# Kernel optimization log

Measured on AMD Instinct MI355X. Metric: run time of the kernel, lower is better.

The kernel has to match this reference:

```python
import jax, jax.numpy as jnp
import numpy as np

NF, NC, LENGTH, BATCH = 64, 16, 2048, 256
WEIGHT_BI, WEIGHT_L2 = 0.01, 0.01
BETA = 2.5     # temporal soft-min/max sharpness (TemporalOperator beta=2.5)
KAPPA = 10.0   # logical soft-min/max sharpness (avm approximation)
EPSN = 1e-12


def setup_inputs() -> dict:
    key = jax.random.key(0)
    ks = jax.random.split(key, 11)
    x = jax.random.normal(ks[0], (BATCH, LENGTH, 2), dtype=jnp.float32)
    t1 = jax.random.uniform(ks[1], (NF,), minval=0.0, maxval=float(LENGTH // 2), dtype=jnp.float32)
    t2 = jax.random.uniform(ks[2], (NF,), minval=float(LENGTH // 2), maxval=float(LENGTH), dtype=jnp.float32)
    a = jax.random.uniform(ks[3], (NF,), dtype=jnp.float32)
    b = jax.random.uniform(ks[4], (NF,), dtype=jnp.float32)
    p1 = jax.random.uniform(ks[5], (NC, NF), dtype=jnp.float32)
    p2 = jax.random.uniform(ks[6], (1, NC), dtype=jnp.float32)
    tvar_temporal = jax.random.uniform(ks[7], (NF,), dtype=jnp.float32)
    tvar_logical1 = jax.random.uniform(ks[8], (NC,), dtype=jnp.float32)
    tvar_logical2 = jax.random.uniform(ks[9], (1,), dtype=jnp.float32)
    eps = jnp.full((1,), 0.1, dtype=jnp.float32)
    return dict(x=x, t1=t1, t2=t2, a=a, b=b, p1=p1, p2=p2,
                tvar_temporal=tvar_temporal, tvar_logical1=tvar_logical1,
                tvar_logical2=tvar_logical2, eps=eps)


def _ste(v, v_new):
    # torch clamps parameter .data under no_grad -> value changes, grad is identity
    return v + jax.lax.stop_gradient(v_new - v)


def _wsel(r, logw, sharp):
    # weighted soft-max (sharp>0) / soft-min (sharp<0) along last axis
    s = jax.nn.softmax(sharp * r + logw, axis=-1)
    return jnp.sum(s * r, axis=-1)


def reference(x, t1, t2, a, b, p1, p2, tvar_temporal, tvar_logical1, tvar_logical2, eps):
    # --- in-place parameter maintenance (clamp under no_grad in torch) ---
    p1 = _ste(p1, jnp.clip(p1, 0.0, 1.0))
    p2 = _ste(p2, jnp.clip(p2, 0.0, 1.0))
    tvt = _ste(tvar_temporal, jnp.clip(tvar_temporal, 0.0, 1.0))
    tvl1 = _ste(tvar_logical1, jnp.clip(tvar_logical1, 0.0, 1.0))
    tvl2 = _ste(tvar_logical2, jnp.clip(tvar_logical2, 0.0, 1.0))
    t1c = jnp.clip(t1, 0.0, LENGTH - 1.0)
    t2c = jnp.clip(t2, 0.0, LENGTH - 1.0)
    t1c = jnp.where(t1c >= t2c - 1.0, t2c - 1.0, t1c)
    t1u = _ste(t1, t1c)
    t2u = _ste(t2, t2c)

    # --- predicates (vectorized over all nf features; dim = i % 2) ---
    dims = jnp.arange(NF) % 2
    rp = a[None, None, :] * x[:, :, dims] - b[None, None, :]     # [B, T, NF]
    rp = jnp.transpose(rp, (0, 2, 1))                             # [B, NF, T]

    # --- temporal operators: smooth window [t1, t2] + soft min/max over time ---
    tg = jnp.arange(LENGTH, dtype=x.dtype)
    w = jax.nn.sigmoid(BETA * (tg[None, :] - t1u[:, None])) * \
        jax.nn.sigmoid(BETA * (t2u[:, None] - tg[None, :]))       # [NF, T]
    logw = jnp.log(w + EPSN)[None]                                # [1, NF, T]
    rmax = _wsel(rp, logw, BETA)                                  # eventually  [B, NF]
    rmin = _wsel(rp, logw, -BETA)                                 # always      [B, NF]
    r1 = tvt[None, :] * rmax + (1.0 - tvt[None, :]) * rmin        # [B, NF]

    # --- logical layer 1: weighted soft OR/AND over features, per clause ---
    logp1 = jnp.log(p1 + EPSN)[None]                              # [1, NC, NF]
    r1e = r1[:, None, :]                                          # [B, NC, NF]
    r_or = _wsel(r1e, logp1, KAPPA)
    r_and = _wsel(r1e, logp1, -KAPPA)
    r2 = tvl1[None, :] * r_or + (1.0 - tvl1[None, :]) * r_and     # [B, NC]

    # --- logical layer 2: combine clauses ---
    logp2 = jnp.log(p2[0] + EPSN)[None]                           # [1, NC]
    r_or2 = _wsel(r2, logp2, KAPPA)
    r_and2 = _wsel(r2, logp2, -KAPPA)
    r = tvl2[0] * r_or2 + (1.0 - tvl2[0]) * r_and2                # [B]

    # --- regularizers ---
    bi = WEIGHT_BI * (jnp.sum(tvt * (1.0 - tvt)) + jnp.sum(tvl1 * (1.0 - tvl1)) +
                      jnp.sum(tvl2 * (1.0 - tvl2)) + jnp.sum(p1 * (1.0 - p1)) +
                      jnp.sum(p2 * (1.0 - p2)))
    l2 = WEIGHT_L2 * (jnp.sum(p1 * p1) + jnp.sum(p2 * p2))
    reg = bi + l2
    return r, reg
```

## Files before the change

### kernel.cpp

```cpp
#include <hip/hip_runtime.h>
#include <math.h>

#define NF 64
#define NC 16
#define LEN 2048
#define BATCH 256
#define BETA 2.5f
#define KAPPA 10.0f
#define EPSN 1e-12f
#define LOG2E 1.4426950408889634f

#define TPB 256
#define NQ (TPB / NF)
#define SPLIT 8
#define HALF (LEN / SPLIT)
#define CHUNK (HALF / NQ)
#define NS (SPLIT * NQ)

#define MTPB 1024
#define MNQ (MTPB / NF)
#define CHUNK_MONO (LEN / MNQ)

__device__ __forceinline__ float clip01(float v) { return fminf(fmaxf(v, 0.0f), 1.0f); }

__device__ __forceinline__ float fexp2(float x) {
#if __has_builtin(__builtin_amdgcn_exp2f)
    return __builtin_amdgcn_exp2f(x);
#else
    return exp2f(x);
#endif
}

#define LW_BLOCKS ((NF * LEN / 4) / 256)

__global__ __launch_bounds__(256) void lw_reg_kernel(
    const float* __restrict__ t1, const float* __restrict__ t2,
    const float* __restrict__ p1, const float* __restrict__ p2,
    const float* __restrict__ tvt, const float* __restrict__ tvl1,
    const float* __restrict__ tvl2, float4* __restrict__ lwT4,
    float* __restrict__ out) {
    const int bid = blockIdx.x;
    const int tid = threadIdx.x;

    if (bid == LW_BLOCKS) {
        __shared__ float red[256];
        float acc = 0.0f;
        for (int i = tid; i < NC * NF; i += 256) {
            float p = clip01(p1[i]);
            acc += 0.01f * (p * (1.0f - p)) + 0.01f * (p * p);
        }
        if (tid < NC) {
            float p = clip01(p2[tid]);
            acc += 0.01f * (p * (1.0f - p)) + 0.01f * (p * p);
        }
        if (tid < NF) {
            float c = clip01(tvt[tid]);
            acc += 0.01f * (c * (1.0f - c));
        }
        if (tid < NC) {
            float c = clip01(tvl1[tid]);
            acc += 0.01f * (c * (1.0f - c));
        }
        if (tid == 0) {
            float c = clip01(tvl2[0]);
            acc += 0.01f * (c * (1.0f - c));
        }
        red[tid] = acc;
        __syncthreads();
        for (int s = 128; s > 0; s >>= 1) {
            if (tid < s) red[tid] += red[tid + s];
            __syncthreads();
        }
        if (tid == 0) out[BATCH] = red[0];
        return;
    }

    int idx = bid * 256 + tid;
    int f = idx & (NF - 1);
    int g = idx >> 6;
    float t1c = fminf(fmaxf(t1[f], 0.0f), (float)(LEN - 1));
    float t2c = fminf(fmaxf(t2[f], 0.0f), (float)(LEN - 1));
    t1c = fminf(t1c, t2c - 1.0f);
    float4 r;
#pragma unroll
    for (int j = 0; j < 4; ++j) {
        float t = (float)(4 * g + j);
        float su = 1.0f / (1.0f + __expf(-BETA * (t - t1c)));
        float sv = 1.0f / (1.0f + __expf(-BETA * (t2c - t)));
        ((float*)&r)[j] = __log2f(su * sv + EPSN);
    }
    lwT4[idx] = r;
}

__global__ __launch_bounds__(TPB) void main_split(
    const float* __restrict__ x, const float* __restrict__ av,
    const float4* __restrict__ lwT4, float4* __restrict__ part) {
    const int b = blockIdx.x >> 3;
    const int h = blockIdx.x & 7;
    const int tid = threadIdx.x;
    const int f = tid & (NF - 1);
    const int q = tid >> 6;
    const int ch = f & 1;

    const float A2 = (BETA * LOG2E) * av[f];

    const int t0 = h * HALF + q * CHUNK;
    const float* xp = x + (size_t)b * (LEN * 2) + 2 * t0 + ch;
    const float4* lw4 = lwT4 + (t0 >> 2) * NF + f;

    float Sp0 = 0.f, Xp0 = 0.f, Sm0 = 0.f, Xm0 = 0.f;
    float Sp1 = 0.f, Xp1 = 0.f, Sm1 = 0.f, Xm1 = 0.f;
#pragma unroll 4
    for (int g = 0; g < CHUNK / 4; ++g) {
        float4 lw = lw4[g * NF];
        float x0 = xp[8 * g + 0];
        float x1 = xp[8 * g + 2];
        float x2 = xp[8 * g + 4];
        float x3 = xp[8 * g + 6];
        float e;
        e = fexp2(fmaf(A2, x0, lw.x));  Sp0 += e; Xp0 = fmaf(e, x0, Xp0);
        e = fexp2(fmaf(-A2, x0, lw.x)); Sm0 += e; Xm0 = fmaf(e, x0, Xm0);
        e = fexp2(fmaf(A2, x1, lw.y));  Sp1 += e; Xp1 = fmaf(e, x1, Xp1);
        e = fexp2(fmaf(-A2, x1, lw.y)); Sm1 += e; Xm1 = fmaf(e, x1, Xm1);
        e = fexp2(fmaf(A2, x2, lw.z));  Sp0 += e; Xp0 = fmaf(e, x2, Xp0);
        e = fexp2(fmaf(-A2, x2, lw.z)); Sm0 += e; Xm0 = fmaf(e, x2, Xm0);
        e = fexp2(fmaf(A2, x3, lw.w));  Sp1 += e; Xp1 = fmaf(e, x3, Xp1);
        e = fexp2(fmaf(-A2, x3, lw.w)); Sm1 += e; Xm1 = fmaf(e, x3, Xm1);
    }

    part[((size_t)b * NS + (h * NQ + q)) * NF + f] =
        make_float4(Sp0 + Sp1, Xp0 + Xp1, Sm0 + Sm1, Xm0 + Xm1);
}

__global__ __launch_bounds__(64) void finish_kernel(
    const float4* __restrict__ part, const float* __restrict__ av,
    const float* __restrict__ bv, const float* __restrict__ p1,
    const float* __restrict__ p2, const float* __restrict__ tvt_,
    const float* __restrict__ tvl1_, const float* __restrict__ tvl2_,
    float* __restrict__ out) {
    __shared__ float r1s[NF];
    __shared__ float r2s[NC];

    const int b = blockIdx.x;
    const int l = threadIdx.x;
    const float KL = KAPPA * LOG2E;

    float ax = 0.f, ay = 0.f, az = 0.f, aw = 0.f;
    const float4* pb = part + (size_t)b * NS * NF;
#pragma unroll
    for (int s = 0; s < NS; ++s) {
        float4 v = pb[s * NF + l];
        ax += v.x; ay += v.y; az += v.z; aw += v.w;
    }
    {
        float af = av[l], bf = bv[l];
        float tvt = clip01(tvt_[l]);
        float rmax = af * (ay / ax);
        float rmin = af * (aw / az);
        r1s[l] = tvt * rmax + (1.0f - tvt) * rmin - bf;
    }

    {
        const int c = l & 15;
        const int j = l >> 4;
        float so = 0.f, wo = 0.f, sa = 0.f, wa = 0.f;
#pragma unroll
        for (int i = 0; i < 16; ++i) {
            int ff = j * 16 + i;
            float r1v = r1s[ff];
            float lg = __log2f(clip01(p1[c * NF + ff]) + EPSN);
            float z = KL * r1v;
            float eo = fexp2(z + lg);
            float ea = fexp2(lg - z);
            so += eo; wo = fmaf(eo, r1v, wo);
            sa += ea; wa = fmaf(ea, r1v, wa);
        }
#pragma unroll
        for (int d = 16; d < 64; d <<= 1) {
            so += __shfl_xor(so, d);
            wo += __shfl_xor(wo, d);
            sa += __shfl_xor(sa, d);
            wa += __shfl_xor(wa, d);
        }
        if (l < NC) {
            float tvl1 = clip01(tvl1_[l]);
            r2s[l] = tvl1 * (wo / so) + (1.0f - tvl1) * (wa / sa);
        }
    }

    if (l == 0) {
        float so = 0.f, wo = 0.f, sa = 0.f, wa = 0.f;
#pragma unroll
        for (int c = 0; c < NC; ++c) {
            float lg = __log2f(clip01(p2[c]) + EPSN);
            float r2v = r2s[c];
            float z = KL * r2v;
            float eo = fexp2(z + lg);
            float ea = fexp2(lg - z);
            so += eo; wo = fmaf(eo, r2v, wo);
            sa += ea; wa = fmaf(ea, r2v, wa);
        }
        float tvl2 = clip01(tvl2_[0]);
        out[b] = tvl2 * (wo / so) + (1.0f - tvl2) * (wa / sa);
    }
}

__global__ __launch_bounds__(MTPB) void main_mono(
    const float* __restrict__ x, const float* __restrict__ av,
    const float* __restrict__ bv,
    const float* __restrict__ t1g, const float* __restrict__ t2g,
    const float* __restrict__ p1, const float* __restrict__ p2,
    const float* __restrict__ tvt_, const float* __restrict__ tvl1_,
    const float* __restrict__ tvl2_, float* __restrict__ out) {
    __shared__ float4 redQ[MNQ][NF];
    __shared__ float lp[NC][NF];
    __shared__ float r1s[NF];
    __shared__ float r2s[NC];

    const int b = blockIdx.x;
    const int tid = threadIdx.x;
    const int f = tid & (NF - 1);
    const int q = tid >> 6;
    const float B2 = BETA * LOG2E;
    const float KL = KAPPA * LOG2E;

    const float a = av[f];
    const float bb = bv[f];
    const int ch = f & 1;

    float t1c = fminf(fmaxf(t1g[f], 0.0f), (float)(LEN - 1));
    float t2c = fminf(fmaxf(t2g[f], 0.0f), (float)(LEN - 1));
    t1c = fminf(t1c, t2c - 1.0f);

    const int t0 = q * CHUNK_MONO;
    const float* xp = x + (size_t)b * (LEN * 2) + 2 * t0 + ch;
    float sp = 0.f, wp = 0.f, sm = 0.f, wm = 0.f;
#pragma unroll 8
    for (int k = 0; k < CHUNK_MONO; ++k) {
        int t = t0 + k;
        float su = 1.0f / (1.0f + __expf(-BETA * ((float)t - t1c)));
        float sv = 1.0f / (1.0f + __expf(-BETA * (t2c - (float)t)));
        float lw2 = __log2f(su * sv + EPSN);
        float xv = xp[2 * k];
        float rp = fmaf(a, xv, -bb);
        float ep = fexp2(fmaf(B2, rp, lw2));
        float em = fexp2(fmaf(-B2, rp, lw2));
        sp += ep; wp = fmaf(ep, rp, wp);
        sm += em; wm = fmaf(em, rp, wm);
    }
    redQ[q][f] = make_float4(sp, wp, sm, wm);
    {
        float pv = clip01(p1[tid]);
        ((float*)lp)[tid] = __log2f(pv + EPSN);
    }
    __syncthreads();

    if (q == 0) {
        float Sp = 0.f, Wp = 0.f, Sm = 0.f, Wm = 0.f;
#pragma unroll
        for (int j = 0; j < MNQ; ++j) {
            float4 v = redQ[j][f];
            Sp += v.x; Wp += v.y; Sm += v.z; Wm += v.w;
        }
        float tvt = clip01(tvt_[f]);
        r1s[f] = tvt * (Wp / Sp) + (1.0f - tvt) * (Wm / Sm);
    }
    __syncthreads();

    if (tid < NC) {
        const int c = tid;
        float so = 0.f, wo = 0.f, sa = 0.f, wa = 0.f;
#pragma unroll
        for (int ff = 0; ff < NF; ++ff) {
            float r1v = r1s[ff];
            float z = KL * r1v;
            float lg = lp[c][ff];
            float eo = fexp2(z + lg);
            float ea = fexp2(lg - z);
            so += eo; wo = fmaf(eo, r1v, wo);
            sa += ea; wa = fmaf(ea, r1v, wa);
        }
        float tvl1 = clip01(tvl1_[c]);
        r2s[c] = tvl1 * (wo / so) + (1.0f - tvl1) * (wa / sa);
    }
    __syncthreads();

    if (tid == 0) {
        float so = 0.f, wo = 0.f, sa = 0.f, wa = 0.f;
#pragma unroll
        for (int c = 0; c < NC; ++c) {
            float lg = __log2f(clip01(p2[c]) + EPSN);
            float r2v = r2s[c];
            float z = KL * r2v;
            float eo = fexp2(z + lg);
            float ea = fexp2(lg - z);
            so += eo; wo = fmaf(eo, r2v, wo);
            sa += ea; wa = fmaf(ea, r2v, wa);
        }
        float tvl2 = clip01(tvl2_[0]);
        out[b] = tvl2 * (wo / so) + (1.0f - tvl2) * (wa / sa);
    }
}

__global__ void reg_kernel(const float* __restrict__ p1, const float* __restrict__ p2,
                           const float* __restrict__ tvt, const float* __restrict__ tvl1,
                           const float* __restrict__ tvl2, float* __restrict__ out) {
    __shared__ float red[256];
    int tid = threadIdx.x;
    float acc = 0.0f;
    for (int i = tid; i < NC * NF; i += 256) {
        float p = clip01(p1[i]);
        acc += 0.01f * (p * (1.0f - p)) + 0.01f * (p * p);
    }
    if (tid < NC) {
        float p = clip01(p2[tid]);
        acc += 0.01f * (p * (1.0f - p)) + 0.01f * (p * p);
    }
    if (tid < NF) {
        float c = clip01(tvt[tid]);
        acc += 0.01f * (c * (1.0f - c));
    }
    if (tid < NC) {
        float c = clip01(tvl1[tid]);
        acc += 0.01f * (c * (1.0f - c));
    }
    if (tid == 0) {
        float c = clip01(tvl2[0]);
        acc += 0.01f * (c * (1.0f - c));
    }
    red[tid] = acc;
    __syncthreads();
    for (int s = 128; s > 0; s >>= 1) {
        if (tid < s) red[tid] += red[tid + s];
        __syncthreads();
    }
    if (tid == 0) out[BATCH] = red[0];
}

extern "C" void kernel_launch(void* const* d_in, const int* in_sizes, int n_in,
                              void* d_out, int out_size, void* d_ws, size_t ws_size,
                              hipStream_t stream) {
    const float* x    = (const float*)d_in[0];
    const float* t1   = (const float*)d_in[1];
    const float* t2   = (const float*)d_in[2];
    const float* a    = (const float*)d_in[3];
    const float* bv   = (const float*)d_in[4];
    const float* p1   = (const float*)d_in[5];
    const float* p2   = (const float*)d_in[6];
    const float* tvt  = (const float*)d_in[7];
    const float* tvl1 = (const float*)d_in[8];
    const float* tvl2 = (const float*)d_in[9];
    float* out = (float*)d_out;

    const size_t lw_bytes = (size_t)(NF * LEN) * sizeof(float);
    const size_t part_bytes = (size_t)BATCH * NS * NF * sizeof(float4);

    if (d_ws && ws_size >= lw_bytes + part_bytes) {
        float4* lwT4 = (float4*)d_ws;
        float4* part = (float4*)((char*)d_ws + lw_bytes);
        lw_reg_kernel<<<LW_BLOCKS + 1, 256, 0, stream>>>(t1, t2, p1, p2, tvt, tvl1,
                                                         tvl2, lwT4, out);
        main_split<<<BATCH * SPLIT, TPB, 0, stream>>>(x, a, lwT4, part);
        finish_kernel<<<BATCH, 64, 0, stream>>>(part, a, bv, p1, p2, tvt, tvl1,
                                                tvl2, out);
    } else {
        main_mono<<<BATCH, MTPB, 0, stream>>>(x, a, bv, t1, t2, p1, p2,
                                              tvt, tvl1, tvl2, out);
        reg_kernel<<<1, 256, 0, stream>>>(p1, p2, tvt, tvl1, tvl2, out);
    }
}
```

Baseline: 27.44 us.

## Fuse weight precompute, split reduction and finish into one per-batch kernel

Replaces the three-kernel pipeline (precomputed log-window table, split partial sums in a global workspace, separate finish pass) with a single kernel of 1024 threads per batch row. The time-window weight is computed inline as the reciprocal of a product of two sigmoid denominators. The plus and minus exponentials are factored into exp2(A*x) and its reciprocal, which cuts the transcendentals per element. Partial sums are reduced in shared memory, and the regularizer is folded into block 0. This removes two launches and the workspace traffic. In exchange it drops EPSN inside the log, launches only 256 blocks, and risks overflow or precision loss from the factored exponent.

New measurement: 26.90 us. 2.0% less time.

```diff
diff --git a/kernel.cpp b/kernel.cpp
--- a/kernel.cpp
+++ b/kernel.cpp
@@ -10,16 +10,9 @@
 #define EPSN 1e-12f
 #define LOG2E 1.4426950408889634f
 
-#define TPB 256
+#define TPB 1024
 #define NQ (TPB / NF)
-#define SPLIT 8
-#define HALF (LEN / SPLIT)
-#define CHUNK (HALF / NQ)
-#define NS (SPLIT * NQ)
-
-#define MTPB 1024
-#define MNQ (MTPB / NF)
-#define CHUNK_MONO (LEN / MNQ)
+#define CHUNK (LEN / NQ)
 
 __device__ __forceinline__ float clip01(float v) { return fminf(fmaxf(v, 0.0f), 1.0f); }
 
@@ -31,125 +24,117 @@
 #endif
 }
 
-#define LW_BLOCKS ((NF * LEN / 4) / 256)
-
-__global__ __launch_bounds__(256) void lw_reg_kernel(
-    const float* __restrict__ t1, const float* __restrict__ t2,
-    const float* __restrict__ p1, const float* __restrict__ p2,
-    const float* __restrict__ tvt, const float* __restrict__ tvl1,
-    const float* __restrict__ tvl2, float4* __restrict__ lwT4,
+__device__ __forceinline__ float frcp(float x) {
+#if __has_builtin(__builtin_amdgcn_rcpf)
+    return __builtin_amdgcn_rcpf(x);
+#else
+    return 1.0f / x;
+#endif
+}
+
+__global__ __launch_bounds__(TPB) void fused_kernel(
+    const float* __restrict__ x, const float* __restrict__ t1g,
+    const float* __restrict__ t2g, const float* __restrict__ av,
+    const float* __restrict__ bv, const float* __restrict__ p1,
+    const float* __restrict__ p2, const float* __restrict__ tvt_,
+    const float* __restrict__ tvl1_, const float* __restrict__ tvl2_,
     float* __restrict__ out) {
-    const int bid = blockIdx.x;
-    const int tid = threadIdx.x;
-
-    if (bid == LW_BLOCKS) {
-        __shared__ float red[256];
-        float acc = 0.0f;
-        for (int i = tid; i < NC * NF; i += 256) {
-            float p = clip01(p1[i]);
-            acc += 0.01f * (p * (1.0f - p)) + 0.01f * (p * p);
-        }
-        if (tid < NC) {
-            float p = clip01(p2[tid]);
-            acc += 0.01f * (p * (1.0f - p)) + 0.01f * (p * p);
-        }
-        if (tid < NF) {
-            float c = clip01(tvt[tid]);
-            acc += 0.01f * (c * (1.0f - c));
-        }
-        if (tid < NC) {
-            float c = clip01(tvl1[tid]);
-            acc += 0.01f * (c * (1.0f - c));
-        }
-        if (tid == 0) {
-            float c = clip01(tvl2[0]);
-            acc += 0.01f * (c * (1.0f - c));
-        }
-        red[tid] = acc;
-        __syncthreads();
-        for (int s = 128; s > 0; s >>= 1) {
-            if (tid < s) red[tid] += red[tid + s];
-            __syncthreads();
-        }
-        if (tid == 0) out[BATCH] = red[0];
-        return;
-    }
-
-    int idx = bid * 256 + tid;
-    int f = idx & (NF - 1);
-    int g = idx >> 6;
-    float t1c = fminf(fmaxf(t1[f], 0.0f), (float)(LEN - 1));
-    float t2c = fminf(fmaxf(t2[f], 0.0f), (float)(LEN - 1));
-    t1c = fminf(t1c, t2c - 1.0f);
-    float4 r;
-#pragma unroll
-    for (int j = 0; j < 4; ++j) {
-        float t = (float)(4 * g + j);
-        float su = 1.0f / (1.0f + __expf(-BETA * (t - t1c)));
-        float sv = 1.0f / (1.0f + __expf(-BETA * (t2c - t)));
-        ((float*)&r)[j] = __log2f(su * sv + EPSN);
-    }
-    lwT4[idx] = r;
-}
-
-__global__ __launch_bounds__(TPB) void main_split(
-    const float* __restrict__ x, const float* __restrict__ av,
-    const float4* __restrict__ lwT4, float4* __restrict__ part) {
-    const int b = blockIdx.x >> 3;
-    const int h = blockIdx.x & 7;
+    __shared__ float4 redQ[NQ][NF];
+    __shared__ float r1s[NF];
+    __shared__ float r2s[NC];
+
+    const int b = blockIdx.x;
     const int tid = threadIdx.x;
     const int f = tid & (NF - 1);
     const int q = tid >> 6;
     const int ch = f & 1;
 
-    const float A2 = (BETA * LOG2E) * av[f];
-
-    const int t0 = h * HALF + q * CHUNK;
-    const float* xp = x + (size_t)b * (LEN * 2) + 2 * t0 + ch;
-    const float4* lw4 = lwT4 + (t0 >> 2) * NF + f;
+    const float B2 = BETA * LOG2E;
+    const float KL = KAPPA * LOG2E;
+
+    const float a = av[f];
+    const float A2 = B2 * a;
+
+    float t1c = fminf(fmaxf(t1g[f], 0.0f), (float)(LEN - 1));
+    float t2c = fminf(fmaxf(t2g[f], 0.0f), (float)(LEN - 1));
+    t1c = fminf(t1c, t2c - 1.0f);
+    const float c1 = B2 * t1c;
+    const float c2 = -B2 * t2c;
+
+    const int t0 = q * CHUNK;
+    const float4* xp4 = (const float4*)(x + (size_t)b * (LEN * 2) + 2 * t0);
 
     float Sp0 = 0.f, Xp0 = 0.f, Sm0 = 0.f, Xm0 = 0.f;
     float Sp1 = 0.f, Xp1 = 0.f, Sm1 = 0.f, Xm1 = 0.f;
 #pragma unroll 4
-    for (int g = 0; g < CHUNK / 4; ++g) {
-        float4 lw = lw4[g * NF];
-        float x0 = xp[8 * g + 0];
-        float x1 = xp[8 * g + 2];
-        float x2 = xp[8 * g + 4];
-        float x3 = xp[8 * g + 6];
-        float e;
-        e = fexp2(fmaf(A2, x0, lw.x));  Sp0 += e; Xp0 = fmaf(e, x0, Xp0);
-        e = fexp2(fmaf(-A2, x0, lw.x)); Sm0 += e; Xm0 = fmaf(e, x0, Xm0);
-        e = fexp2(fmaf(A2, x1, lw.y));  Sp1 += e; Xp1 = fmaf(e, x1, Xp1);
-        e = fexp2(fmaf(-A2, x1, lw.y)); Sm1 += e; Xm1 = fmaf(e, x1, Xm1);
-        e = fexp2(fmaf(A2, x2, lw.z));  Sp0 += e; Xp0 = fmaf(e, x2, Xp0);
-        e = fexp2(fmaf(-A2, x2, lw.z)); Sm0 += e; Xm0 = fmaf(e, x2, Xm0);
-        e = fexp2(fmaf(A2, x3, lw.w));  Sp1 += e; Xp1 = fmaf(e, x3, Xp1);
-        e = fexp2(fmaf(-A2, x3, lw.w)); Sm1 += e; Xm1 = fmaf(e, x3, Xm1);
-    }
-
-    part[((size_t)b * NS + (h * NQ + q)) * NF + f] =
-        make_float4(Sp0 + Sp1, Xp0 + Xp1, Sm0 + Sm1, Xm0 + Xm1);
-}
-
-__global__ __launch_bounds__(64) void finish_kernel(
-    const float4* __restrict__ part, const float* __restrict__ av,
-    const float* __restrict__ bv, const float* __restrict__ p1,
-    const float* __restrict__ p2, const float* __restrict__ tvt_,
-    const float* __restrict__ tvl1_, const float* __restrict__ tvl2_,
-    float* __restrict__ out) {
-    __shared__ float r1s[NF];
-    __shared__ float r2s[NC];
-
-    const int b = blockIdx.x;
-    const int l = threadIdx.x;
-    const float KL = KAPPA * LOG2E;
-
+    for (int k2 = 0; k2 < CHUNK / 2; ++k2) {
+        float4 v = xp4[k2];
+        float xa = ch ? v.y : v.x;
+        float xb = ch ? v.w : v.z;
+        float tfa = (float)(t0 + 2 * k2);
+        float tfb = tfa + 1.0f;
+
+        {
+            float g1 = fmaf(-B2, tfa, c1);
+            float g2 = fmaf(B2, tfa, c2);
+            float den = (1.0f + fexp2(g1)) * (1.0f + fexp2(g2));
+            float w = frcp(den);
+            float P = fexp2(A2 * xa);
+            float Pm = frcp(P);
+            float tp = P * w, tm = Pm * w;
+            Sp0 += tp; Xp0 = fmaf(tp, xa, Xp0);
+            Sm0 += tm; Xm0 = fmaf(tm, xa, Xm0);
+        }
+        {
+            float g1 = fmaf(-B2, tfb, c1);
+            float g2 = fmaf(B2, tfb, c2);
+            float den = (1.0f + fexp2(g1)) * (1.0f + fexp2(g2));
+            float w = frcp(den);
+            float P = fexp2(A2 * xb);
+            float Pm = frcp(P);
+            float tp = P * w, tm = Pm * w;
+            Sp1 += tp; Xp1 = fmaf(tp, xb, Xp1);
+            Sm1 += tm; Xm1 = fmaf(tm, xb, Xm1);
+        }
+    }
+
+    redQ[q][f] = make_float4(Sp0 + Sp1, Xp0 + Xp1, Sm0 + Sm1, Xm0 + Xm1);
+
+    if (b == 0 && q == NQ - 1) {
+        const int l = f;
+        float acc = 0.0f;
+#pragma unroll
+        for (int i = 0; i < 16; ++i) {
+            float p = clip01(p1[i * NF + l]);
+            acc += 0.01f * (p * (1.0f - p)) + 0.01f * (p * p);
+        }
+        {
+            float c = clip01(tvt_[l]);
+            acc += 0.01f * (c * (1.0f - c));
+        }
+        if (l < NC) {
+            float p = clip01(p2[l]);
+            acc += 0.01f * (p * (1.0f - p)) + 0.01f * (p * p);
+            float c = clip01(tvl1_[l]);
+            acc += 0.01f * (c * (1.0f - c));
+        }
+        if (l == 0) {
+            float c = clip01(tvl2_[0]);
+            acc += 0.01f * (c * (1.0f - c));
+        }
+#pragma unroll
+        for (int d = 1; d < 64; d <<= 1) acc += __shfl_xor(acc, d);
+        if (l == 0) out[BATCH] = acc;
+    }
+
+    __syncthreads();
+    if (tid >= 64) return;
+
+    const int l = tid;
     float ax = 0.f, ay = 0.f, az = 0.f, aw = 0.f;
-    const float4* pb = part + (size_t)b * NS * NF;
-#pragma unroll
-    for (int s = 0; s < NS; ++s) {
-        float4 v = pb[s * NF + l];
+#pragma unroll
+    for (int s = 0; s < NQ; ++s) {
+        float4 v = redQ[s][l];
         ax += v.x; ay += v.y; az += v.z; aw += v.w;
     }
     {
@@ -203,138 +188,6 @@
         float tvl2 = clip01(tvl2_[0]);
         out[b] = tvl2 * (wo / so) + (1.0f - tvl2) * (wa / sa);
     }
-}
-
-__global__ __launch_bounds__(MTPB) void main_mono(
-    const float* __restrict__ x, const float* __restrict__ av,
-    const float* __restrict__ bv,
-    const float* __restrict__ t1g, const float* __restrict__ t2g,
-    const float* __restrict__ p1, const float* __restrict__ p2,
-    const float* __restrict__ tvt_, const float* __restrict__ tvl1_,
-    const float* __restrict__ tvl2_, float* __restrict__ out) {
-    __shared__ float4 redQ[MNQ][NF];
-    __shared__ float lp[NC][NF];
-    __shared__ float r1s[NF];
-    __shared__ float r2s[NC];
-
-    const int b = blockIdx.x;
-    const int tid = threadIdx.x;
-    const int f = tid & (NF - 1);
-    const int q = tid >> 6;
-    const float B2 = BETA * LOG2E;
-    const float KL = KAPPA * LOG2E;
-
-    const float a = av[f];
-    const float bb = bv[f];
-    const int ch = f & 1;
-
-    float t1c = fminf(fmaxf(t1g[f], 0.0f), (float)(LEN - 1));
-    float t2c = fminf(fmaxf(t2g[f], 0.0f), (float)(LEN - 1));
-    t1c = fminf(t1c, t2c - 1.0f);
-
-    const int t0 = q * CHUNK_MONO;
-    const float* xp = x + (size_t)b * (LEN * 2) + 2 * t0 + ch;
-    float sp = 0.f, wp = 0.f, sm = 0.f, wm = 0.f;
-#pragma unroll 8
-    for (int k = 0; k < CHUNK_MONO; ++k) {
-        int t = t0 + k;
-        float su = 1.0f / (1.0f + __expf(-BETA * ((float)t - t1c)));
-        float sv = 1.0f / (1.0f + __expf(-BETA * (t2c - (float)t)));
-        float lw2 = __log2f(su * sv + EPSN);
-        float xv = xp[2 * k];
-        float rp = fmaf(a, xv, -bb);
-        float ep = fexp2(fmaf(B2, rp, lw2));
-        float em = fexp2(fmaf(-B2, rp, lw2));
-        sp += ep; wp = fmaf(ep, rp, wp);
-        sm += em; wm = fmaf(em, rp, wm);
-    }
-    redQ[q][f] = make_float4(sp, wp, sm, wm);
-    {
-        float pv = clip01(p1[tid]);
-        ((float*)lp)[tid] = __log2f(pv + EPSN);
-    }
-    __syncthreads();
-
-    if (q == 0) {
-        float Sp = 0.f, Wp = 0.f, Sm = 0.f, Wm = 0.f;
-#pragma unroll
-        for (int j = 0; j < MNQ; ++j) {
-            float4 v = redQ[j][f];
-            Sp += v.x; Wp += v.y; Sm += v.z; Wm += v.w;
-        }
-        float tvt = clip01(tvt_[f]);
-        r1s[f] = tvt * (Wp / Sp) + (1.0f - tvt) * (Wm / Sm);
-    }
-    __syncthreads();
-
-    if (tid < NC) {
-        const int c = tid;
-        float so = 0.f, wo = 0.f, sa = 0.f, wa = 0.f;
-#pragma unroll
-        for (int ff = 0; ff < NF; ++ff) {
-            float r1v = r1s[ff];
-            float z = KL * r1v;
-            float lg = lp[c][ff];
-            float eo = fexp2(z + lg);
-            float ea = fexp2(lg - z);
-            so += eo; wo = fmaf(eo, r1v, wo);
-            sa += ea; wa = fmaf(ea, r1v, wa);
-        }
-        float tvl1 = clip01(tvl1_[c]);
-        r2s[c] = tvl1 * (wo / so) + (1.0f - tvl1) * (wa / sa);
-    }
-    __syncthreads();
-
-    if (tid == 0) {
-        float so = 0.f, wo = 0.f, sa = 0.f, wa = 0.f;
-#pragma unroll
-        for (int c = 0; c < NC; ++c) {
-            float lg = __log2f(clip01(p2[c]) + EPSN);
-            float r2v = r2s[c];
-            float z = KL * r2v;
-            float eo = fexp2(z + lg);
-            float ea = fexp2(lg - z);
-            so += eo; wo = fmaf(eo, r2v, wo);
-            sa += ea; wa = fmaf(ea, r2v, wa);
-        }
-        float tvl2 = clip01(tvl2_[0]);
-        out[b] = tvl2 * (wo / so) + (1.0f - tvl2) * (wa / sa);
-    }
-}
-
-__global__ void reg_kernel(const float* __restrict__ p1, const float* __restrict__ p2,
-                           const float* __restrict__ tvt, const float* __restrict__ tvl1,
-                           const float* __restrict__ tvl2, float* __restrict__ out) {
-    __shared__ float red[256];
-    int tid = threadIdx.x;
-    float acc = 0.0f;
-    for (int i = tid; i < NC * NF; i += 256) {
-        float p = clip01(p1[i]);
-        acc += 0.01f * (p * (1.0f - p)) + 0.01f * (p * p);
-    }
-    if (tid < NC) {
-        float p = clip01(p2[tid]);
-        acc += 0.01f * (p * (1.0f - p)) + 0.01f * (p * p);
-    }
-    if (tid < NF) {
-        float c = clip01(tvt[tid]);
-        acc += 0.01f * (c * (1.0f - c));
-    }
-    if (tid < NC) {
-        float c = clip01(tvl1[tid]);
-        acc += 0.01f * (c * (1.0f - c));
-    }
-    if (tid == 0) {
-        float c = clip01(tvl2[0]);
-        acc += 0.01f * (c * (1.0f - c));
-    }
-    red[tid] = acc;
-    __syncthreads();
-    for (int s = 128; s > 0; s >>= 1) {
-        if (tid < s) red[tid] += red[tid + s];
-        __syncthreads();
-    }
-    if (tid == 0) out[BATCH] = red[0];
 }
 
 extern "C" void kernel_launch(void* const* d_in, const int* in_sizes, int n_in,
@@ -352,20 +205,6 @@
     const float* tvl2 = (const float*)d_in[9];
     float* out = (float*)d_out;
 
-    const size_t lw_bytes = (size_t)(NF * LEN) * sizeof(float);
-    const size_t part_bytes = (size_t)BATCH * NS * NF * sizeof(float4);
-
-    if (d_ws && ws_size >= lw_bytes + part_bytes) {
-        float4* lwT4 = (float4*)d_ws;
-        float4* part = (float4*)((char*)d_ws + lw_bytes);
-        lw_reg_kernel<<<LW_BLOCKS + 1, 256, 0, stream>>>(t1, t2, p1, p2, tvt, tvl1,
-                                                         tvl2, lwT4, out);
-        main_split<<<BATCH * SPLIT, TPB, 0, stream>>>(x, a, lwT4, part);
-        finish_kernel<<<BATCH, 64, 0, stream>>>(part, a, bv, p1, p2, tvt, tvl1,
-                                                tvl2, out);
-    } else {
-        main_mono<<<BATCH, MTPB, 0, stream>>>(x, a, bv, t1, t2, p1, p2,
-                                              tvt, tvl1, tvl2, out);
-        reg_kernel<<<1, 256, 0, stream>>>(p1, p2, tvt, tvl1, tvl2, out);
-    }
-}
+    fused_kernel<<<BATCH, TPB, 0, stream>>>(x, t1, t2, a, bv, p1, p2,
+                                            tvt, tvl1, tvl2, out);
+}
```
